# Kernel tuning notes

Measured on AMD Instinct MI355X. Metric: run time of the kernel, lower is better.

## Reference

```python
import jax, jax.numpy as jnp
import numpy as np

DECAY = 0.8
EPS = 1e-05


def setup_inputs() -> dict:
    key = jax.random.key(0)
    k1, k2, k3 = jax.random.split(key, 3)
    b, n, d = 16, 4096, 64
    h, c = 1, 2048
    x = jax.random.normal(k1, (b, n, d), dtype=jnp.float32)
    embeddings = jax.random.normal(k2, (h, c, d), dtype=jnp.float32)
    cluster_size = jnp.ones((h, c), dtype=jnp.float32)
    embed_avg = jax.random.normal(k3, (h, c, d), dtype=jnp.float32)
    return {"x": x, "embeddings": embeddings, "cluster_size": cluster_size, "embed_avg": embed_avg}


def reference(x, embeddings, cluster_size, embed_avg):
    # x: (b, n, d); add codebook dim h=1 and flatten -> (h, N, d)
    d = x.shape[-1]
    flat = x.reshape(1, -1, d)                              # (h, N, d)
    h, C = embeddings.shape[0], embeddings.shape[1]

    # dist = -cdist(flat, embeddings)  (negative euclidean distance)
    x2 = jnp.sum(flat * flat, axis=-1, keepdims=True)       # (h, N, 1)
    e2 = jnp.sum(embeddings * embeddings, axis=-1)          # (h, C)
    xe = jnp.einsum('hnd,hcd->hnc', flat, embeddings)       # (h, N, C)
    dist = -jnp.sqrt(jnp.clip(x2 + e2[:, None, :] - 2.0 * xe, 0.0))

    # gumbel_sample with stochastic=False, straight_through=False -> hard argmax
    embed_ind = jnp.argmax(dist, axis=-1)                   # (h, N)

    # quantize: gather selected codes
    quantize = jnp.take_along_axis(embeddings, embed_ind[..., None], axis=1)  # (h, N, d)

    # EMA codebook update (scatter-based): counts and per-code feature sums
    counts = jax.vmap(lambda i: jnp.bincount(i, length=C))(embed_ind).astype(x.dtype)  # (h, C)
    embed_sum = jax.vmap(lambda f, i: jax.ops.segment_sum(f, i, num_segments=C))(flat, embed_ind)  # (h, C, d)

    new_cluster_size = cluster_size * DECAY + counts * (1.0 - DECAY)
    new_embed_avg = embed_avg * DECAY + embed_sum * (1.0 - DECAY)

    # laplace smoothing of cluster sizes, then renormalize embed_avg
    tot = jnp.sum(new_cluster_size, axis=-1, keepdims=True)
    smoothed = (new_cluster_size + EPS) / (tot + C * EPS) * tot
    new_embeddings = new_embed_avg / smoothed[..., None]

    quantize = quantize.reshape(x.shape)                    # drop h dim back to (b, n, d)
    embed_ind = embed_ind.reshape(x.shape[:-1])             # (b, n)
    return quantize, embed_ind, new_embeddings, new_cluster_size, new_embed_avg
```

## Files before the change

kernel.cpp:

```cpp
#include <hip/hip_runtime.h>

#define N_TOK 65536
#define D 64
#define C_CODES 2048
#define DECAYF 0.8f
#define OMDF 0.2f
#define EPSF 1e-5f
#define SEG 16
#define GAP_THR 0.0625f
#define TCODES 64
#define HT (1024 / TCODES)

#define OUT_QUANT 0
#define OUT_IND   (N_TOK * D)
#define OUT_EMB   (OUT_IND + N_TOK)
#define OUT_CS    (OUT_EMB + C_CODES * D)
#define OUT_EAVG  (OUT_CS + C_CODES)

typedef short s16x8 __attribute__((ext_vector_type(8)));
typedef float f32x4 __attribute__((ext_vector_type(4)));

__device__ __forceinline__ unsigned short f2bf(float f) {
    unsigned int u = __float_as_uint(f);
    return (unsigned short)((u + 0x7fffu + ((u >> 16) & 1u)) >> 16);
}
__device__ __forceinline__ float bf2f(unsigned short h) {
    return __uint_as_float(((unsigned int)h) << 16);
}
__device__ __forceinline__ unsigned long long shflx64w(unsigned long long v, int mask, int w) {
    unsigned int lo = (unsigned int)v, hi = (unsigned int)(v >> 32);
    lo = __shfl_xor(lo, mask, w);
    hi = __shfl_xor(hi, mask, w);
    return ((unsigned long long)hi << 32) | lo;
}
__device__ __forceinline__ void gload_lds16(const void* g, void* l) {
    __builtin_amdgcn_global_load_lds(
        (const __attribute__((address_space(1))) void*)g,
        (__attribute__((address_space(3))) void*)l, 16, 0, 0);
}

__device__ __forceinline__ void merge3(
        float a1, unsigned int ca1, float a2, unsigned int ca2, float a3,
        float b1, unsigned int cb1, float b2, unsigned int cb2, float b3,
        float& m1, unsigned int& cm1, float& m2, unsigned int& cm2, float& m3) {
    bool ta = a1 <= b1;
    m1 = ta ? a1 : b1;
    cm1 = ta ? ca1 : cb1;
    float x1v = ta ? b1 : a1;
    unsigned int xc = ta ? cb1 : ca1;
    bool tb = a2 <= b2;
    float y1v = tb ? a2 : b2;
    unsigned int yc = tb ? ca2 : cb2;
    bool tc = x1v <= y1v;
    m2 = tc ? x1v : y1v;
    cm2 = tc ? xc : yc;
    m3 = fminf(fmaxf(x1v, y1v), fminf(a3, b3));
}

__global__ void eprep_kernel(const float* __restrict__ emb, short* __restrict__ ebk,
                             float* __restrict__ e2, unsigned int* __restrict__ e2p,
                             float* __restrict__ counts, float* __restrict__ embed_sum,
                             int* __restrict__ pend_n) {
    int g = blockIdx.x * blockDim.x + threadIdx.x;
    int code = g >> 3, slot = g & 7;
    int kc = slot ^ (code & 7);
    const float4* ep = (const float4*)(emb + (size_t)code * D + kc * 8);
    float4 a = ep[0], b = ep[1];
    float v[8] = {a.x, a.y, a.z, a.w, b.x, b.y, b.z, b.w};
    s16x8 h, l;
#pragma unroll
    for (int j = 0; j < 8; ++j) {
        unsigned short hb = f2bf(v[j]);
        h[j] = (short)hb;
        l[j] = (short)f2bf(v[j] - bf2f(hb));
    }
    *(s16x8*)(ebk + (size_t)code * 128 + slot * 8) = h;
    *(s16x8*)(ebk + (size_t)code * 128 + 64 + slot * 8) = l;

    float4 z = {0.f, 0.f, 0.f, 0.f};
    ((float4*)embed_sum)[g * 2] = z;
    ((float4*)embed_sum)[g * 2 + 1] = z;
    if (g < C_CODES / 4) ((float4*)counts)[g] = z;
    if (g == 0) pend_n[0] = 0;

    if (g < C_CODES) {
        const float4* er = (const float4*)(emb + (size_t)g * D);
        float s0 = 0.f, s1 = 0.f, s2 = 0.f, s3 = 0.f;
#pragma unroll
        for (int i = 0; i < D / 4; ++i) {
            float4 e = er[i];
            s0 = fmaf(e.x, e.x, s0);
            s1 = fmaf(e.y, e.y, s1);
            s2 = fmaf(e.z, e.z, s2);
            s3 = fmaf(e.w, e.w, s3);
        }
        float vv = (s0 + s1) + (s2 + s3);
        e2[g] = vv;
        unsigned short hb = f2bf(vv);
        unsigned short lb = f2bf(vv - bf2f(hb));
        e2p[g] = (unsigned int)hb | ((unsigned int)lb << 16);
    }
}

__global__ __launch_bounds__(256) void screen_kernel(
        const float* __restrict__ x, const short* __restrict__ ebk,
        const unsigned int* __restrict__ e2p, uint4* __restrict__ ktop2,
        float* __restrict__ kb3) {
    __shared__ unsigned int e2pl[1024];
    __shared__ __align__(16) char bstage[2][TCODES * 256];

    const int tid = threadIdx.x;
    const int bh = blockIdx.y;
    ((uint4*)e2pl)[tid] = ((const uint4*)(e2p + bh * 1024))[tid];

    const int lane = tid & 63;
    const int wave = tid >> 6;
    const int col = lane & 15;
    const int krow = lane >> 4;

    s16x8 ah[2][2], al[2][2];
#pragma unroll
    for (int s = 0; s < 2; ++s) {
        int tok = blockIdx.x * 128 + wave * 32 + s * 16 + col;
        const float4* xp = (const float4*)(x + (size_t)tok * D + krow * 8);
        float4 f0 = xp[0], f1 = xp[1], f2 = xp[8], f3 = xp[9];
        float xv[16] = {f0.x, f0.y, f0.z, f0.w, f1.x, f1.y, f1.z, f1.w,
                        f2.x, f2.y, f2.z, f2.w, f3.x, f3.y, f3.z, f3.w};
#pragma unroll
        for (int j = 0; j < 8; ++j) {
            float v0 = -2.0f * xv[j];
            unsigned short h0 = f2bf(v0);
            ah[s][0][j] = (short)h0;
            al[s][0][j] = (short)f2bf(v0 - bf2f(h0));
            float v1 = -2.0f * xv[8 + j];
            unsigned short h1 = f2bf(v1);
            ah[s][1][j] = (short)h1;
            al[s][1][j] = (short)f2bf(v1 - bf2f(h1));
        }
    }

    s16x8 aone = {0, 0, 0, 0, 0, 0, 0, 0};
    {
        short o = (krow == 0) ? (short)0x3F80 : (short)0;
        aone[0] = o;
        aone[1] = o;
    }
    const f32x4 zero = {0.f, 0.f, 0.f, 0.f};

    float b1[2][4], b2[2][4], b3[2][4];
    unsigned int c1[2][4], c2[2][4];
#pragma unroll
    for (int s = 0; s < 2; ++s)
#pragma unroll
        for (int r = 0; r < 4; ++r) {
            b1[s][r] = __builtin_inff();
            b2[s][r] = __builtin_inff();
            b3[s][r] = __builtin_inff();
            c1[s][r] = 0u;
            c2[s][r] = 0u;
        }

    auto stage = [&](int b, int t) {
        const char* src = (const char*)ebk + (size_t)(bh * HT + t) * (TCODES * 256)
                          + wave * 4096 + lane * 16;
        char* dst = &bstage[b][wave * 4096];
        gload_lds16(src, dst);
        gload_lds16(src + 1024, dst + 1024);
        gload_lds16(src + 2048, dst + 2048);
        gload_lds16(src + 3072, dst + 3072);
    };

    auto subtile = [&](const char* lb, int t, int j) {
        const char* base = lb + (j << 12) + (col << 8);
        int off = (krow ^ (col & 7)) << 4;
        s16x8 bh0 = *(const s16x8*)(base + off);
        s16x8 bh1 = *(const s16x8*)(base + (off ^ 64));
        s16x8 bl0 = *(const s16x8*)(base + 128 + off);
        s16x8 bl1 = *(const s16x8*)(base + 128 + (off ^ 64));
        int sloc = t * 4 + j;
        unsigned int cg = (unsigned int)(bh * 1024 + sloc * 16 + col);
        unsigned int v = e2pl[sloc * 16 + col];
        v = (krow == 0) ? v : 0u;
        s16x8 be2 = {(short)(v & 0xffffu), (short)(v >> 16), 0, 0, 0, 0, 0, 0};
        f32x4 f = __builtin_amdgcn_mfma_f32_16x16x32_bf16(aone, be2, zero, 0, 0, 0);
#pragma unroll
        for (int s = 0; s < 2; ++s) {
            f32x4 acc = __builtin_amdgcn_mfma_f32_16x16x32_bf16(ah[s][1], bh1, f, 0, 0, 0);
            acc = __builtin_amdgcn_mfma_f32_16x16x32_bf16(ah[s][0], bh0, acc, 0, 0, 0);
            acc = __builtin_amdgcn_mfma_f32_16x16x32_bf16(al[s][1], bh1, acc, 0, 0, 0);
            acc = __builtin_amdgcn_mfma_f32_16x16x32_bf16(al[s][0], bh0, acc, 0, 0, 0);
            acc = __builtin_amdgcn_mfma_f32_16x16x32_bf16(ah[s][1], bl1, acc, 0, 0, 0);
            acc = __builtin_amdgcn_mfma_f32_16x16x32_bf16(ah[s][0], bl0, acc, 0, 0, 0);
#pragma unroll
            for (int r = 0; r < 4; ++r) {
                float sc = acc[r];
                bool l1 = sc < b1[s][r];
                bool l2 = sc < b2[s][r];
                b3[s][r] = __builtin_amdgcn_fmed3f(b2[s][r], b3[s][r], sc);
                b2[s][r] = __builtin_amdgcn_fmed3f(b1[s][r], b2[s][r], sc);
                unsigned int tc = l1 ? c1[s][r] : cg;
                c2[s][r] = l2 ? tc : c2[s][r];
                b1[s][r] = fminf(b1[s][r], sc);
                c1[s][r] = l1 ? cg : c1[s][r];
            }
        }
    };

    stage(0, 0);
    __syncthreads();

    for (int t = 0; t < HT; ++t) {
        if (t + 1 < HT) stage((t + 1) & 1, t + 1);
        const char* lb = bstage[t & 1];
        subtile(lb, t, 0);
        subtile(lb, t, 1);
        subtile(lb, t, 2);
        subtile(lb, t, 3);
        __syncthreads();
    }

#pragma unroll
    for (int s = 0; s < 2; ++s)
#pragma unroll
        for (int r = 0; r < 4; ++r) {
            float B1 = b1[s][r], B2 = b2[s][r], B3 = b3[s][r];
            unsigned int C1 = c1[s][r], C2 = c2[s][r];
#pragma unroll
            for (int mk = 1; mk < 16; mk <<= 1) {
                float o1 = __shfl_xor(B1, mk, 16);
                float o2 = __shfl_xor(B2, mk, 16);
                float o3 = __shfl_xor(B3, mk, 16);
                unsigned int oc1 = (unsigned int)__shfl_xor((int)C1, mk, 16);
                unsigned int oc2 = (unsigned int)__shfl_xor((int)C2, mk, 16);
                float nm1, nm2, nm3;
                unsigned int nc1, nc2;
                merge3(B1, C1, B2, C2, B3, o1, oc1, o2, oc2, o3,
                       nm1, nc1, nm2, nc2, nm3);
                B1 = nm1; C1 = nc1; B2 = nm2; C2 = nc2; B3 = nm3;
            }
            if (col == 0) {
                int tok = blockIdx.x * 128 + wave * 32 + s * 16 + krow * 4 + r;
                uint4 o;
                o.x = __float_as_uint(B1);
                o.y = C1;
                o.z = __float_as_uint(B2);
                o.w = C2;
                ktop2[(size_t)tok * 2 + bh] = o;
                kb3[(size_t)tok * 2 + bh] = B3;
            }
        }
}

__global__ __launch_bounds__(256) void merge_kernel(
        const float* __restrict__ x, const float* __restrict__ emb,
        const float* __restrict__ e2, const uint4* __restrict__ ktop2,
        const float* __restrict__ kb3,
        int* __restrict__ idx, float* __restrict__ out, float* __restrict__ counts,
        int* __restrict__ pend_n, unsigned int* __restrict__ pend) {
    int n = blockIdx.x * blockDim.x + threadIdx.x;

    uint4 A = ktop2[(size_t)n * 2];
    uint4 B = ktop2[(size_t)n * 2 + 1];
    float a3 = kb3[(size_t)n * 2], b3v = kb3[(size_t)n * 2 + 1];
    float m1, m2, m3;
    unsigned int cm1u, cm2u;
    merge3(__uint_as_float(A.x), A.y, __uint_as_float(A.z), A.w, a3,
           __uint_as_float(B.x), B.y, __uint_as_float(B.z), B.w, b3v,
           m1, cm1u, m2, cm2u, m3);

    int c = (int)cm1u;
    bool uniq = (m2 - m1 > GAP_THR);
    bool pairf = !uniq && (m3 - m1 > GAP_THR);

    if (pairf) {
        int ca = c, cb = (int)cm2u;
        float xs[4] = {0.f, 0.f, 0.f, 0.f};
        float da[4] = {0.f, 0.f, 0.f, 0.f};
        float db[4] = {0.f, 0.f, 0.f, 0.f};
        for (int q = 0; q < 4; ++q) {
            const float4* xq = (const float4*)(x + (size_t)n * D + q * 16);
            const float4* ea = (const float4*)(emb + (size_t)ca * D + q * 16);
            const float4* eb = (const float4*)(emb + (size_t)cb * D + q * 16);
#pragma unroll
            for (int j = 0; j < 4; ++j) {
                float4 xv = xq[j], av = ea[j], bv = eb[j];
                xs[0] = fmaf(xv.x, xv.x, xs[0]);
                xs[1] = fmaf(xv.y, xv.y, xs[1]);
                xs[2] = fmaf(xv.z, xv.z, xs[2]);
                xs[3] = fmaf(xv.w, xv.w, xs[3]);
                da[0] = fmaf(xv.x, av.x, da[0]);
                da[1] = fmaf(xv.y, av.y, da[1]);
                da[2] = fmaf(xv.z, av.z, da[2]);
                da[3] = fmaf(xv.w, av.w, da[3]);
                db[0] = fmaf(xv.x, bv.x, db[0]);
                db[1] = fmaf(xv.y, bv.y, db[1]);
                db[2] = fmaf(xv.z, bv.z, db[2]);
                db[3] = fmaf(xv.w, bv.w, db[3]);
            }
        }
        float x2 = (xs[0] + xs[1]) + (xs[2] + xs[3]);
        float dota = (da[0] + da[1]) + (da[2] + da[3]);
        float dA = fmaxf(x2 + e2[ca] - 2.0f * dota, 0.0f);
        float dotb = (db[0] + db[1]) + (db[2] + db[3]);
        float dB = fmaxf(x2 + e2[cb] - 2.0f * dotb, 0.0f);
        unsigned long long ka = ((unsigned long long)__float_as_uint(dA) << 32) | (unsigned int)ca;
        unsigned long long kb = ((unsigned long long)__float_as_uint(dB) << 32) | (unsigned int)cb;
        c = (int)((ka < kb ? ka : kb) & 0xffffffffull);
    }

    if (uniq || pairf) {
        idx[n] = c;
        out[OUT_IND + n] = (float)c;
        atomicAdd(&counts[c], 1.0f);
    } else {
        int p = atomicAdd(pend_n, 1);
        if (p >= 0 && p < N_TOK) pend[p] = (unsigned int)n;
    }
}

__global__ __launch_bounds__(256) void cleanup_kernel(
        const float* __restrict__ x, const float* __restrict__ emb,
        const float* __restrict__ e2, const int* __restrict__ pend_n,
        const unsigned int* __restrict__ pend,
        int* __restrict__ idx, float* __restrict__ out, float* __restrict__ counts) {
    int gw = (int)((blockIdx.x * blockDim.x + threadIdx.x) >> 6);
    int nw = (int)((gridDim.x * blockDim.x) >> 6);
    int lane = threadIdx.x & 63;
    int M = pend_n[0];
    M = (M < 0) ? 0 : ((M > N_TOK) ? N_TOK : M);
    for (int i = gw; i < M; i += nw) {
        int tn = (int)(pend[i] & 0xffffu);
        float xs[4] = {0.f, 0.f, 0.f, 0.f};
        for (int q = 0; q < 4; ++q) {
            const float4* xq = (const float4*)(x + (size_t)tn * D + q * 16);
#pragma unroll
            for (int j = 0; j < 4; ++j) {
                float4 xv = xq[j];
                xs[0] = fmaf(xv.x, xv.x, xs[0]);
                xs[1] = fmaf(xv.y, xv.y, xs[1]);
                xs[2] = fmaf(xv.z, xv.z, xs[2]);
                xs[3] = fmaf(xv.w, xv.w, xs[3]);
            }
        }
        float tx2 = (xs[0] + xs[1]) + (xs[2] + xs[3]);
        unsigned long long kbest = ~0ull;
        for (int cc = lane; cc < C_CODES; cc += 64) {
            float d0 = 0.f, d1 = 0.f, d2 = 0.f, d3 = 0.f;
            for (int q = 0; q < 4; ++q) {
                const float4* xq = (const float4*)(x + (size_t)tn * D + q * 16);
                const float4* er = (const float4*)(emb + (size_t)cc * D + q * 16);
#pragma unroll
                for (int j = 0; j < 4; ++j) {
                    float4 xv = xq[j], ev = er[j];
                    d0 = fmaf(xv.x, ev.x, d0);
                    d1 = fmaf(xv.y, ev.y, d1);
                    d2 = fmaf(xv.z, ev.z, d2);
                    d3 = fmaf(xv.w, ev.w, d3);
                }
            }
            float dot = (d0 + d1) + (d2 + d3);
            float dist2 = fmaxf(tx2 + e2[cc] - 2.0f * dot, 0.0f);
            unsigned long long key =
                ((unsigned long long)__float_as_uint(dist2) << 32) | (unsigned int)cc;
            kbest = key < kbest ? key : kbest;
        }
#pragma unroll
        for (int mk = 1; mk < 64; mk <<= 1) {
            unsigned long long o = shflx64w(kbest, mk, 64);
            kbest = o < kbest ? o : kbest;
        }
        if (lane == 0) {
            int c = (int)(kbest & 0xffffffffull);
            idx[tn] = c;
            out[OUT_IND + tn] = (float)c;
            atomicAdd(&counts[c], 1.0f);
        }
    }
}

__global__ void gather_kernel(const float* __restrict__ emb,
                              const int* __restrict__ idx,
                              float* __restrict__ out) {
    int g = blockIdx.x * blockDim.x + threadIdx.x;
    int n = g >> 4;
    int j = g & 15;
    int c = idx[n];
    float4 e = ((const float4*)emb)[c * (D / 4) + j];
    ((float4*)(out + OUT_QUANT))[g] = e;
}

__global__ void prefix_ema_kernel(const float* __restrict__ counts,
                                  const float* __restrict__ cluster_size,
                                  float* __restrict__ out,
                                  float* __restrict__ smoothed,
                                  int* __restrict__ cursor) {
    __shared__ float scan[256];
    __shared__ float red[256];
    int t = threadIdx.x;
    int base = t * 8;
    float cnt[8], ncs[8];
    float csum = 0.f, nsum = 0.f;
#pragma unroll
    for (int j = 0; j < 8; ++j) {
        cnt[j] = counts[base + j];
        csum += cnt[j];
        ncs[j] = cluster_size[base + j] * DECAYF + cnt[j] * OMDF;
        nsum += ncs[j];
        out[OUT_CS + base + j] = ncs[j];
    }
    scan[t] = csum;
    red[t] = nsum;
    __syncthreads();
    for (int s = 1; s < 256; s <<= 1) {
        float v = scan[t];
        float w = (t >= s) ? scan[t - s] : 0.f;
        __syncthreads();
        scan[t] = v + w;
        __syncthreads();
    }
    for (int s = 128; s > 0; s >>= 1) {
        if (t < s) red[t] += red[t + s];
        __syncthreads();
    }
    float tot = red[0];
    float run = (t == 0) ? 0.f : scan[t - 1];
#pragma unroll
    for (int j = 0; j < 8; ++j) {
        cursor[base + j] = (int)run;
        run += cnt[j];
        smoothed[base + j] = (ncs[j] + EPSF) / (tot + (float)C_CODES * EPSF) * tot;
    }
}

__global__ void scatter_pos_kernel(const int* __restrict__ idx,
                                   int* __restrict__ cursor,
                                   unsigned int* __restrict__ sorted) {
    int n = blockIdx.x * blockDim.x + threadIdx.x;
    int c = idx[n];
    int pos = atomicAdd(&cursor[c], 1);
    sorted[pos] = ((unsigned int)c << 16) | (unsigned int)n;
}

__global__ __launch_bounds__(256) void seg_sum_kernel(
        const float* __restrict__ x, const unsigned int* __restrict__ sorted,
        float* __restrict__ embed_sum) {
    int lane = threadIdx.x & 63;
    int q = blockIdx.x * 4 + (threadIdx.x >> 6);
    int p0 = q * SEG;

    unsigned int mine = (lane < SEG) ? sorted[p0 + lane] : 0u;
    unsigned int pk[SEG];
#pragma unroll
    for (int j = 0; j < SEG; ++j) pk[j] = __shfl(mine, j, 64);

    float xv[SEG];
#pragma unroll
    for (int j = 0; j < SEG; ++j)
        xv[j] = x[(size_t)(pk[j] & 0xffffu) * D + lane];

    unsigned int run_c = 0xffffffffu;
    float sum = 0.f;
#pragma unroll
    for (int j = 0; j < SEG; ++j) {
        unsigned int c = pk[j] >> 16;
        if (c != run_c) {
            if (run_c != 0xffffffffu)
                atomicAdd(&embed_sum[(size_t)run_c * D + lane], sum);
            run_c = c;
            sum = 0.f;
        }
        sum += xv[j];
    }
    atomicAdd(&embed_sum[(size_t)run_c * D + lane], sum);
}

__global__ void ema_embed_kernel(const float* __restrict__ embed_avg,
                                 const float* __restrict__ embed_sum,
                                 const float* __restrict__ smoothed,
                                 float* __restrict__ out) {
    int g = blockIdx.x * blockDim.x + threadIdx.x;
    int c = g >> 4;
    float4 ea = ((const float4*)embed_avg)[g];
    float4 es = ((const float4*)embed_sum)[g];
    float4 na;
    na.x = ea.x * DECAYF + es.x * OMDF;
    na.y = ea.y * DECAYF + es.y * OMDF;
    na.z = ea.z * DECAYF + es.z * OMDF;
    na.w = ea.w * DECAYF + es.w * OMDF;
    ((float4*)(out + OUT_EAVG))[g] = na;
    float sm = smoothed[c];
    float4 ne;
    ne.x = na.x / sm;
    ne.y = na.y / sm;
    ne.z = na.z / sm;
    ne.w = na.w / sm;
    ((float4*)(out + OUT_EMB))[g] = ne;
}

extern "C" void kernel_launch(void* const* d_in, const int* in_sizes, int n_in,
                              void* d_out, int out_size, void* d_ws, size_t ws_size,
                              hipStream_t stream) {
    const float* x            = (const float*)d_in[0];
    const float* emb          = (const float*)d_in[1];
    const float* cluster_size = (const float*)d_in[2];
    const float* embed_avg    = (const float*)d_in[3];
    float* out = (float*)d_out;

    float* e2        = (float*)d_ws;
    unsigned int* e2p = (unsigned int*)(e2 + C_CODES);
    float* counts    = (float*)(e2p + C_CODES);
    float* smoothed  = counts + C_CODES;
    int*   cursor    = (int*)(smoothed + C_CODES);
    int*   idx       = cursor + C_CODES;
    unsigned int* sorted = (unsigned int*)(idx + N_TOK);
    int*   pend_n    = (int*)(sorted + N_TOK);
    unsigned int* pend = (unsigned int*)(pend_n + 4);
    uint4* ktop2     = (uint4*)(pend + N_TOK);
    float* kb3       = (float*)(ktop2 + (size_t)N_TOK * 2);
    float* embed_sum = kb3 + (size_t)N_TOK * 2;
    short* ebk       = (short*)(embed_sum + C_CODES * D);

    eprep_kernel<<<(C_CODES * 8) / 256, 256, 0, stream>>>(emb, ebk, e2, e2p, counts,
                                                          embed_sum, pend_n);
    screen_kernel<<<dim3(N_TOK / 128, 2), 256, 0, stream>>>(x, ebk, e2p, ktop2, kb3);
    merge_kernel<<<N_TOK / 256, 256, 0, stream>>>(x, emb, e2, ktop2, kb3, idx, out,
                                                  counts, pend_n, pend);
    cleanup_kernel<<<128, 256, 0, stream>>>(x, emb, e2, pend_n, pend, idx, out, counts);
    gather_kernel<<<(N_TOK * 16) / 256, 256, 0, stream>>>(emb, idx, out);
    prefix_ema_kernel<<<1, 256, 0, stream>>>(counts, cluster_size, out, smoothed, cursor);
    scatter_pos_kernel<<<N_TOK / 256, 256, 0, stream>>>(idx, cursor, sorted);
    seg_sum_kernel<<<(N_TOK / SEG) / 4, 256, 0, stream>>>(x, sorted, embed_sum);
    ema_embed_kernel<<<(C_CODES * 16) / 256, 256, 0, stream>>>(embed_avg, embed_sum,
                                                              smoothed, out);
}
```

Before: 279.8 us.

## Fuse merge, cleanup and gather into one exact kernel; add e2 in FP32

Merges the merge, pending-list cleanup and gather kernels into a single exact_kernel that runs 4 threads per token. Ambiguous tokens are handled in-wave through a ballot loop instead of a global pending queue, and the codebook rows are gathered directly into the quantize output. The screen kernel now adds the code norm as a plain FP32 add rather than an extra MFMA with bf16-split norms. This removes two launches, the atomic pending queue and an idx round trip. In exchange, the full 2048-code scans now run inside the wave that owns the token, so a wave with several ambiguous tokens stalls all of its lanes while they are processed.

```diff
diff --git a/kernel.cpp b/kernel.cpp
--- a/kernel.cpp
+++ b/kernel.cpp
@@ -58,9 +58,8 @@
 }
 
 __global__ void eprep_kernel(const float* __restrict__ emb, short* __restrict__ ebk,
-                             float* __restrict__ e2, unsigned int* __restrict__ e2p,
-                             float* __restrict__ counts, float* __restrict__ embed_sum,
-                             int* __restrict__ pend_n) {
+                             float* __restrict__ e2,
+                             float* __restrict__ counts, float* __restrict__ embed_sum) {
     int g = blockIdx.x * blockDim.x + threadIdx.x;
     int code = g >> 3, slot = g & 7;
     int kc = slot ^ (code & 7);
@@ -81,7 +80,6 @@
     ((float4*)embed_sum)[g * 2] = z;
     ((float4*)embed_sum)[g * 2 + 1] = z;
     if (g < C_CODES / 4) ((float4*)counts)[g] = z;
-    if (g == 0) pend_n[0] = 0;
 
     if (g < C_CODES) {
         const float4* er = (const float4*)(emb + (size_t)g * D);
@@ -94,24 +92,20 @@
             s2 = fmaf(e.z, e.z, s2);
             s3 = fmaf(e.w, e.w, s3);
         }
-        float vv = (s0 + s1) + (s2 + s3);
-        e2[g] = vv;
-        unsigned short hb = f2bf(vv);
-        unsigned short lb = f2bf(vv - bf2f(hb));
-        e2p[g] = (unsigned int)hb | ((unsigned int)lb << 16);
+        e2[g] = (s0 + s1) + (s2 + s3);
     }
 }
 
 __global__ __launch_bounds__(256) void screen_kernel(
         const float* __restrict__ x, const short* __restrict__ ebk,
-        const unsigned int* __restrict__ e2p, uint4* __restrict__ ktop2,
+        const float* __restrict__ e2, uint4* __restrict__ ktop2,
         float* __restrict__ kb3) {
-    __shared__ unsigned int e2pl[1024];
+    __shared__ float e2sl[1024];
     __shared__ __align__(16) char bstage[2][TCODES * 256];
 
     const int tid = threadIdx.x;
     const int bh = blockIdx.y;
-    ((uint4*)e2pl)[tid] = ((const uint4*)(e2p + bh * 1024))[tid];
+    ((float4*)e2sl)[tid] = ((const float4*)(e2 + bh * 1024))[tid];
 
     const int lane = tid & 63;
     const int wave = tid >> 6;
@@ -139,12 +133,6 @@
         }
     }
 
-    s16x8 aone = {0, 0, 0, 0, 0, 0, 0, 0};
-    {
-        short o = (krow == 0) ? (short)0x3F80 : (short)0;
-        aone[0] = o;
-        aone[1] = o;
-    }
     const f32x4 zero = {0.f, 0.f, 0.f, 0.f};
 
     float b1[2][4], b2[2][4], b3[2][4];
@@ -179,13 +167,10 @@
         s16x8 bl1 = *(const s16x8*)(base + 128 + (off ^ 64));
         int sloc = t * 4 + j;
         unsigned int cg = (unsigned int)(bh * 1024 + sloc * 16 + col);
-        unsigned int v = e2pl[sloc * 16 + col];
-        v = (krow == 0) ? v : 0u;
-        s16x8 be2 = {(short)(v & 0xffffu), (short)(v >> 16), 0, 0, 0, 0, 0, 0};
-        f32x4 f = __builtin_amdgcn_mfma_f32_16x16x32_bf16(aone, be2, zero, 0, 0, 0);
+        float e2v = e2sl[sloc * 16 + col];
 #pragma unroll
         for (int s = 0; s < 2; ++s) {
-            f32x4 acc = __builtin_amdgcn_mfma_f32_16x16x32_bf16(ah[s][1], bh1, f, 0, 0, 0);
+            f32x4 acc = __builtin_amdgcn_mfma_f32_16x16x32_bf16(ah[s][1], bh1, zero, 0, 0, 0);
             acc = __builtin_amdgcn_mfma_f32_16x16x32_bf16(ah[s][0], bh0, acc, 0, 0, 0);
             acc = __builtin_amdgcn_mfma_f32_16x16x32_bf16(al[s][1], bh1, acc, 0, 0, 0);
             acc = __builtin_amdgcn_mfma_f32_16x16x32_bf16(al[s][0], bh0, acc, 0, 0, 0);
@@ -193,7 +178,7 @@
             acc = __builtin_amdgcn_mfma_f32_16x16x32_bf16(ah[s][0], bl0, acc, 0, 0, 0);
 #pragma unroll
             for (int r = 0; r < 4; ++r) {
-                float sc = acc[r];
+                float sc = acc[r] + e2v;
                 bool l1 = sc < b1[s][r];
                 bool l2 = sc < b2[s][r];
                 b3[s][r] = __builtin_amdgcn_fmed3f(b2[s][r], b3[s][r], sc);
@@ -251,13 +236,16 @@
         }
 }
 
-__global__ __launch_bounds__(256) void merge_kernel(
+__global__ __launch_bounds__(256) void exact_kernel(
         const float* __restrict__ x, const float* __restrict__ emb,
         const float* __restrict__ e2, const uint4* __restrict__ ktop2,
         const float* __restrict__ kb3,
-        int* __restrict__ idx, float* __restrict__ out, float* __restrict__ counts,
-        int* __restrict__ pend_n, unsigned int* __restrict__ pend) {
-    int n = blockIdx.x * blockDim.x + threadIdx.x;
+        int* __restrict__ idx, float* __restrict__ out,
+        float* __restrict__ counts) {
+    int g = blockIdx.x * blockDim.x + threadIdx.x;
+    int n = g >> 2;
+    int q = g & 3;
+    int lane = threadIdx.x & 63;
 
     uint4 A = ktop2[(size_t)n * 2];
     uint4 B = ktop2[(size_t)n * 2 + 1];
@@ -271,16 +259,17 @@
     int c = (int)cm1u;
     bool uniq = (m2 - m1 > GAP_THR);
     bool pairf = !uniq && (m3 - m1 > GAP_THR);
-
-    if (pairf) {
+    bool fullf = !uniq && !pairf;
+
+    if (pairf && q == 0) {
         int ca = c, cb = (int)cm2u;
         float xs[4] = {0.f, 0.f, 0.f, 0.f};
         float da[4] = {0.f, 0.f, 0.f, 0.f};
         float db[4] = {0.f, 0.f, 0.f, 0.f};
-        for (int q = 0; q < 4; ++q) {
-            const float4* xq = (const float4*)(x + (size_t)n * D + q * 16);
-            const float4* ea = (const float4*)(emb + (size_t)ca * D + q * 16);
-            const float4* eb = (const float4*)(emb + (size_t)cb * D + q * 16);
+        for (int qq = 0; qq < 4; ++qq) {
+            const float4* xq = (const float4*)(x + (size_t)n * D + qq * 16);
+            const float4* ea = (const float4*)(emb + (size_t)ca * D + qq * 16);
+            const float4* eb = (const float4*)(emb + (size_t)cb * D + qq * 16);
 #pragma unroll
             for (int j = 0; j < 4; ++j) {
                 float4 xv = xq[j], av = ea[j], bv = eb[j];
@@ -308,31 +297,14 @@
         c = (int)((ka < kb ? ka : kb) & 0xffffffffull);
     }
 
-    if (uniq || pairf) {
-        idx[n] = c;
-        out[OUT_IND + n] = (float)c;
-        atomicAdd(&counts[c], 1.0f);
-    } else {
-        int p = atomicAdd(pend_n, 1);
-        if (p >= 0 && p < N_TOK) pend[p] = (unsigned int)n;
-    }
-}
-
-__global__ __launch_bounds__(256) void cleanup_kernel(
-        const float* __restrict__ x, const float* __restrict__ emb,
-        const float* __restrict__ e2, const int* __restrict__ pend_n,
-        const unsigned int* __restrict__ pend,
-        int* __restrict__ idx, float* __restrict__ out, float* __restrict__ counts) {
-    int gw = (int)((blockIdx.x * blockDim.x + threadIdx.x) >> 6);
-    int nw = (int)((gridDim.x * blockDim.x) >> 6);
-    int lane = threadIdx.x & 63;
-    int M = pend_n[0];
-    M = (M < 0) ? 0 : ((M > N_TOK) ? N_TOK : M);
-    for (int i = gw; i < M; i += nw) {
-        int tn = (int)(pend[i] & 0xffffu);
+    unsigned long long bal = __ballot(fullf && q == 0);
+    while (bal) {
+        int src = (int)__ffsll((long long)bal) - 1;
+        bal &= bal - 1;
+        int tn = __shfl(n, src, 64);
         float xs[4] = {0.f, 0.f, 0.f, 0.f};
-        for (int q = 0; q < 4; ++q) {
-            const float4* xq = (const float4*)(x + (size_t)tn * D + q * 16);
+        for (int qq = 0; qq < 4; ++qq) {
+            const float4* xq = (const float4*)(x + (size_t)tn * D + qq * 16);
 #pragma unroll
             for (int j = 0; j < 4; ++j) {
                 float4 xv = xq[j];
@@ -346,9 +318,9 @@
         unsigned long long kbest = ~0ull;
         for (int cc = lane; cc < C_CODES; cc += 64) {
             float d0 = 0.f, d1 = 0.f, d2 = 0.f, d3 = 0.f;
-            for (int q = 0; q < 4; ++q) {
-                const float4* xq = (const float4*)(x + (size_t)tn * D + q * 16);
-                const float4* er = (const float4*)(emb + (size_t)cc * D + q * 16);
+            for (int qq = 0; qq < 4; ++qq) {
+                const float4* xq = (const float4*)(x + (size_t)tn * D + qq * 16);
+                const float4* er = (const float4*)(emb + (size_t)cc * D + qq * 16);
 #pragma unroll
                 for (int j = 0; j < 4; ++j) {
                     float4 xv = xq[j], ev = er[j];
@@ -369,24 +341,25 @@
             unsigned long long o = shflx64w(kbest, mk, 64);
             kbest = o < kbest ? o : kbest;
         }
-        if (lane == 0) {
-            int c = (int)(kbest & 0xffffffffull);
-            idx[tn] = c;
-            out[OUT_IND + tn] = (float)c;
-            atomicAdd(&counts[c], 1.0f);
-        }
-    }
-}
-
-__global__ void gather_kernel(const float* __restrict__ emb,
-                              const int* __restrict__ idx,
-                              float* __restrict__ out) {
-    int g = blockIdx.x * blockDim.x + threadIdx.x;
-    int n = g >> 4;
-    int j = g & 15;
-    int c = idx[n];
-    float4 e = ((const float4*)emb)[c * (D / 4) + j];
-    ((float4*)(out + OUT_QUANT))[g] = e;
+        if (lane == src) c = (int)(kbest & 0xffffffffull);
+    }
+
+    c = __shfl(c, lane & ~3, 64);
+
+    if (q == 0) {
+        idx[n] = c;
+        out[OUT_IND + n] = (float)c;
+        atomicAdd(&counts[c], 1.0f);
+    }
+
+    {
+        const float4* er = (const float4*)(emb + (size_t)c * D) + q * 4;
+        float4* qo = (float4*)(out + OUT_QUANT) + (size_t)n * 16 + q * 4;
+        qo[0] = er[0];
+        qo[1] = er[1];
+        qo[2] = er[2];
+        qo[3] = er[3];
+    }
 }
 
 __global__ void prefix_ema_kernel(const float* __restrict__ counts,
@@ -507,26 +480,21 @@
     float* out = (float*)d_out;
 
     float* e2        = (float*)d_ws;
-    unsigned int* e2p = (unsigned int*)(e2 + C_CODES);
-    float* counts    = (float*)(e2p + C_CODES);
+    float* counts    = e2 + C_CODES;
     float* smoothed  = counts + C_CODES;
     int*   cursor    = (int*)(smoothed + C_CODES);
     int*   idx       = cursor + C_CODES;
     unsigned int* sorted = (unsigned int*)(idx + N_TOK);
-    int*   pend_n    = (int*)(sorted + N_TOK);
-    unsigned int* pend = (unsigned int*)(pend_n + 4);
-    uint4* ktop2     = (uint4*)(pend + N_TOK);
+    uint4* ktop2     = (uint4*)(sorted + N_TOK);
     float* kb3       = (float*)(ktop2 + (size_t)N_TOK * 2);
     float* embed_sum = kb3 + (size_t)N_TOK * 2;
     short* ebk       = (short*)(embed_sum + C_CODES * D);
 
-    eprep_kernel<<<(C_CODES * 8) / 256, 256, 0, stream>>>(emb, ebk, e2, e2p, counts,
-                                                          embed_sum, pend_n);
-    screen_kernel<<<dim3(N_TOK / 128, 2), 256, 0, stream>>>(x, ebk, e2p, ktop2, kb3);
-    merge_kernel<<<N_TOK / 256, 256, 0, stream>>>(x, emb, e2, ktop2, kb3, idx, out,
-                                                  counts, pend_n, pend);
-    cleanup_kernel<<<128, 256, 0, stream>>>(x, emb, e2, pend_n, pend, idx, out, counts);
-    gather_kernel<<<(N_TOK * 16) / 256, 256, 0, stream>>>(emb, idx, out);
+    eprep_kernel<<<(C_CODES * 8) / 256, 256, 0, stream>>>(emb, ebk, e2, counts,
+                                                          embed_sum);
+    screen_kernel<<<dim3(N_TOK / 128, 2), 256, 0, stream>>>(x, ebk, e2, ktop2, kb3);
+    exact_kernel<<<(N_TOK * 4) / 256, 256, 0, stream>>>(x, emb, e2, ktop2, kb3,
+                                                        idx, out, counts);
     prefix_ema_kernel<<<1, 256, 0, stream>>>(counts, cluster_size, out, smoothed, cursor);
     scatter_pos_kernel<<<N_TOK / 256, 256, 0, stream>>>(idx, cursor, sorted);
     seg_sum_kernel<<<(N_TOK / SEG) / 4, 256, 0, stream>>>(x, sorted, embed_sum);
```

Result: faster. 262.7 us (-6.1%).
